# Kernel tuning notes

Measured on AMD Instinct MI355X. Metric: run time of the kernel, lower is better.

Reference implementation:

```python
import jax, jax.numpy as jnp
import numpy as np

B, C, H, W = 32, 3, 128, 128
OH, OW = 32, 32
N = OH * OW


def calc_mask(mu_x, mu_y, sigma_x, sigma_y):
    # Gaussian receptive-field mask, normalized per neuron over (C,H,W) and
    # rescaled by sqrt(C*H*W), as in AdaptiveLocal2DLayer.calc_U (channel_separate=False,
    # normed=True). The mask is identical across channels, so we keep it [H,W,N]
    # and fold the channel count C into the normalization.
    xg = jnp.linspace(0.0, 1.0, W)
    yg = jnp.linspace(0.0, 1.0, H)
    gx = jnp.exp(-0.5 * ((xg[:, None] - mu_x[None, :]) / sigma_x[None, :]) ** 2)  # [W,N]
    gy = jnp.exp(-0.5 * ((yg[:, None] - mu_y[None, :]) / sigma_y[None, :]) ** 2)  # [H,N]
    g = gy[:, None, :] * gx[None, :, :]  # [H,W,N]
    sumsq = C * jnp.sum(g * g, axis=(0, 1), keepdims=True)  # per-neuron sum over C,H,W
    return g / jnp.sqrt(sumsq) * jnp.sqrt(jnp.asarray(C * H * W, dtype=g.dtype))


def setup_inputs() -> dict:
    key = jax.random.key(0)
    kx, kw = jax.random.split(key)
    x = jax.random.normal(kx, (B, C, H, W), dtype=jnp.float32)
    # mu_init='spread': grid of centers with margin 0.2 (np.meshgrid default 'xy')
    margin = 0.2
    grid_y, grid_x = jnp.meshgrid(
        jnp.linspace(margin, 1.0 - margin, OH),
        jnp.linspace(margin, 1.0 - margin, OW),
        indexing='xy')
    mu_x = grid_x.flatten().astype(jnp.float32)
    mu_y = grid_y.flatten().astype(jnp.float32)
    sigma_x = jnp.full((N,), 0.1, dtype=jnp.float32)
    sigma_y = jnp.full((N,), 0.1, dtype=jnp.float32)
    # weight init as in the module: uniform(-bound, bound) with
    # bound = gain*sqrt(6/(eff_fan_in + fan_out)), eff_fan_in = sum(mask^2)
    mask = calc_mask(mu_x, mu_y, sigma_x, sigma_y)
    eff_fan_in = C * jnp.sum(mask ** 2)
    gain = float(np.sqrt(2.0))  # calculate_gain('relu')
    bound = gain * jnp.sqrt(6.0 / (eff_fan_in + N))
    weights = jax.random.uniform(kw, (C, H, W, N), minval=-bound, maxval=bound,
                                 dtype=jnp.float32)
    return {"x": x, "mu_x": mu_x, "mu_y": mu_y,
            "sigma_x": sigma_x, "sigma_y": sigma_y, "weights": weights}


def reference(x, mu_x, mu_y, sigma_x, sigma_y, weights):
    # forward: weighted_mask = mask * weights; tensordot over (C,H,W)
    mask = calc_mask(mu_x, mu_y, sigma_x, sigma_y)  # [H,W,N]
    wm = mask[None, :, :, :] * weights               # [C,H,W,N]
    out = jnp.einsum('bchw,chwn->bn', x, wm)         # [B,N]
    return out.reshape(x.shape[0], 1, OH, OW)
```

## Files before the change

kernel.cpp:

```cpp
#include <hip/hip_runtime.h>
#include <stdint.h>

#define BB 32
#define CC 3
#define HH 128
#define WW 128
#define NN 1024
#define KK (CC*HH*WW)
#define NROWS (CC*HH)
#define KSR NROWS
#define BH 16
#define BSPLIT (BB/BH)
#define NF4 (NN/4)
#define WCH 4
#define NCH (WW/WCH)
#define STEP (1.0f/127.0f)

__global__ void scale_kernel(const float* __restrict__ mu_x,
                             const float* __restrict__ mu_y,
                             const float* __restrict__ sigma_x,
                             const float* __restrict__ sigma_y,
                             float* __restrict__ scale) {
    int n = blockIdx.x * blockDim.x + threadIdx.x;
    if (n >= NN) return;
    float mux = mu_x[n], muy = mu_y[n];
    float isx = 1.0f / sigma_x[n], isy = 1.0f / sigma_y[n];
    float Sx = 0.f, Sy = 0.f;
    for (int i = 0; i < WW; ++i) {
        float dx = (i * STEP - mux) * isx;
        Sx += __expf(-dx * dx);
        float dy = (i * STEP - muy) * isy;
        Sy += __expf(-dy * dy);
    }
    scale[n] = sqrtf((float)(HH * WW) / (Sx * Sy));
}

__global__ void table_kernel(const float* __restrict__ mu_x,
                             const float* __restrict__ mu_y,
                             const float* __restrict__ sigma_x,
                             const float* __restrict__ sigma_y,
                             const float* __restrict__ scale,
                             float* __restrict__ gxt,
                             float* __restrict__ gyt) {
    int id = blockIdx.x * blockDim.x + threadIdx.x;
    int n = id & (NN - 1);
    int i = id >> 10;
    float sx = sigma_x[n], sy = sigma_y[n];
    float dx = i * STEP - mu_x[n];
    float dy = i * STEP - mu_y[n];
    gxt[id] = __expf(-0.5f * dx * dx / (sx * sx));
    gyt[id] = __expf(-0.5f * dy * dy / (sy * sy)) * scale[n];
}

__global__ __launch_bounds__(256) void main_pipe(
    const float* __restrict__ weights,
    const float* __restrict__ x,
    const float* __restrict__ gyt,
    const float* __restrict__ mu_x,
    const float* __restrict__ sigma_x,
    float* __restrict__ part)
{
    __shared__ float wbuf[2][WCH * NN];
    __shared__ float xtile[WW][BH];
    const int tid = threadIdx.x;

    const int d    = blockIdx.x;
    const int xcd  = d & 7;
    const int slot = d >> 3;
    const int g    = xcd * (KSR / 8) + (slot >> 1);
    const int b0   = (slot & 1) * BH;
    const int r    = g;
    const int h    = r & (HH - 1);

    {
        const int b = tid & (BH - 1);
        const int c = tid >> 4;
        const float* xp = x + (size_t)(b0 + b) * KK + (size_t)r * WW + c * 8;
        const float4 v0 = ((const float4*)xp)[0];
        const float4 v1 = ((const float4*)xp)[1];
        const int w = c * 8;
        xtile[w+0][b] = v0.x; xtile[w+1][b] = v0.y;
        xtile[w+2][b] = v0.z; xtile[w+3][b] = v0.w;
        xtile[w+4][b] = v1.x; xtile[w+5][b] = v1.y;
        xtile[w+6][b] = v1.z; xtile[w+7][b] = v1.w;
    }

    const float4 mux = ((const float4*)mu_x)[tid];
    const float4 sx  = ((const float4*)sigma_x)[tid];
    float4 ax, axs, Bf;
    ax.x = -0.5f/(sx.x*sx.x); ax.y = -0.5f/(sx.y*sx.y);
    ax.z = -0.5f/(sx.z*sx.z); ax.w = -0.5f/(sx.w*sx.w);
    axs.x = ax.x*STEP; axs.y = ax.y*STEP; axs.z = ax.z*STEP; axs.w = ax.w*STEP;
    Bf.x = __expf(2.f*axs.x*STEP); Bf.y = __expf(2.f*axs.y*STEP);
    Bf.z = __expf(2.f*axs.z*STEP); Bf.w = __expf(2.f*axs.w*STEP);

    const float4 gyrow = ((const float4*)(gyt + (size_t)h * NN))[tid];

    auto stage = [&](int c) {
        const int w0 = c * WCH;
        const float* gsrc = weights + ((size_t)r * WW + w0) * NN;
        float* lb = wbuf[c & 1];
        const int q = tid >> 6;
        const int lane = tid & 63;
#pragma unroll
        for (int i = 0; i < 4; ++i) {
            const int off = q * 1024 + i * 256;
            __builtin_amdgcn_global_load_lds(
                (const __attribute__((address_space(1))) unsigned int*)(gsrc + off + lane * 4),
                (__attribute__((address_space(3))) unsigned int*)(lb + off),
                16, 0, 0);
        }
    };

    stage(0);
    __syncthreads();

    float4 acc[BH];
#pragma unroll
    for (int b = 0; b < BH; ++b) acc[b] = make_float4(0.f, 0.f, 0.f, 0.f);

    for (int c = 0; c < NCH; ++c) {
        if (c + 1 < NCH) stage(c + 1);

        const int w0 = c * WCH;
        float4 g4, r4;
        {
            float dd;
            dd = w0*STEP - mux.x; g4.x = __expf(ax.x*dd*dd)*gyrow.x; r4.x = __expf(axs.x*(2.f*dd+STEP));
            dd = w0*STEP - mux.y; g4.y = __expf(ax.y*dd*dd)*gyrow.y; r4.y = __expf(axs.y*(2.f*dd+STEP));
            dd = w0*STEP - mux.z; g4.z = __expf(ax.z*dd*dd)*gyrow.z; r4.z = __expf(axs.z*(2.f*dd+STEP));
            dd = w0*STEP - mux.w; g4.w = __expf(ax.w*dd*dd)*gyrow.w; r4.w = __expf(axs.w*(2.f*dd+STEP));
        }

        const float* wb = wbuf[c & 1];
#pragma unroll
        for (int i = 0; i < WCH; ++i) {
            const float4 wt = *(const float4*)(wb + i * NN + (tid << 2));
            const float4* tr = (const float4*)&xtile[w0 + i][0];
            float4 t;
            t.x = g4.x * wt.x; t.y = g4.y * wt.y;
            t.z = g4.z * wt.z; t.w = g4.w * wt.w;
#pragma unroll
            for (int q = 0; q < 4; ++q) {
                const float4 xv = tr[q];
                acc[4*q+0].x = fmaf(xv.x, t.x, acc[4*q+0].x);
                acc[4*q+0].y = fmaf(xv.x, t.y, acc[4*q+0].y);
                acc[4*q+0].z = fmaf(xv.x, t.z, acc[4*q+0].z);
                acc[4*q+0].w = fmaf(xv.x, t.w, acc[4*q+0].w);
                acc[4*q+1].x = fmaf(xv.y, t.x, acc[4*q+1].x);
                acc[4*q+1].y = fmaf(xv.y, t.y, acc[4*q+1].y);
                acc[4*q+1].z = fmaf(xv.y, t.z, acc[4*q+1].z);
                acc[4*q+1].w = fmaf(xv.y, t.w, acc[4*q+1].w);
                acc[4*q+2].x = fmaf(xv.z, t.x, acc[4*q+2].x);
                acc[4*q+2].y = fmaf(xv.z, t.y, acc[4*q+2].y);
                acc[4*q+2].z = fmaf(xv.z, t.z, acc[4*q+2].z);
                acc[4*q+2].w = fmaf(xv.z, t.w, acc[4*q+2].w);
                acc[4*q+3].x = fmaf(xv.w, t.x, acc[4*q+3].x);
                acc[4*q+3].y = fmaf(xv.w, t.y, acc[4*q+3].y);
                acc[4*q+3].z = fmaf(xv.w, t.z, acc[4*q+3].z);
                acc[4*q+3].w = fmaf(xv.w, t.w, acc[4*q+3].w);
            }
            g4.x *= r4.x; g4.y *= r4.y; g4.z *= r4.z; g4.w *= r4.w;
            r4.x *= Bf.x; r4.y *= Bf.y; r4.z *= Bf.z; r4.w *= Bf.w;
        }
        __syncthreads();
    }

    float* pp = part + ((size_t)g * BB + b0) * NN + (tid << 2);
#pragma unroll
    for (int b = 0; b < BH; ++b)
        *(float4*)(pp + (size_t)b * NN) = acc[b];
}

template <int KSS>
__global__ __launch_bounds__(256) void reduce_kernel(const float* __restrict__ part,
                                                     float* __restrict__ out) {
    __shared__ float buf[256];
    const int t = threadIdx.x;
    const int half = t >> 7;
    const int cell = blockIdx.x * 128 + (t & 127);
    const int s0 = half * (KSS / 2);
    float a = 0.f;
#pragma unroll 8
    for (int s = 0; s < KSS / 2; ++s)
        a += part[(size_t)(s0 + s) * (BB * NN) + cell];
    buf[t] = a;
    __syncthreads();
    if (t < 128) out[cell] = buf[t] + buf[t + 128];
}

template <int MODE>
__global__ __launch_bounds__(256) void main_fallback(
    const float* __restrict__ weights,
    const float* __restrict__ x,
    const float* __restrict__ gxt,
    const float* __restrict__ gyt,
    const float* __restrict__ mu_x, const float* __restrict__ mu_y,
    const float* __restrict__ sigma_x, const float* __restrict__ sigma_y,
    float* __restrict__ dst)
{
    __shared__ float tile[2][WW][8];
    const int tid = threadIdx.x;
    const int g   = blockIdx.x;
    const int b0  = blockIdx.y * 8;
    const int r0  = g * 2;

    {
        const int b = tid & 7;
        const int c = tid >> 3;
        const float* xp = x + (size_t)(b0 + b) * KK + (size_t)r0 * WW + c * 8;
        const float4 v0 = ((const float4*)xp)[0];
        const float4 v1 = ((const float4*)xp)[1];
        const int row = (c * 8) >> 7;
        const int w   = (c * 8) & (WW - 1);
        tile[row][w+0][b] = v0.x; tile[row][w+1][b] = v0.y;
        tile[row][w+2][b] = v0.z; tile[row][w+3][b] = v0.w;
        tile[row][w+4][b] = v1.x; tile[row][w+5][b] = v1.y;
        tile[row][w+6][b] = v1.z; tile[row][w+7][b] = v1.w;
    }

    float4 mux4, ax4, ay4, muy4, sc4;
    if constexpr (MODE == 2) {
        mux4 = ((const float4*)mu_x)[tid];
        muy4 = ((const float4*)mu_y)[tid];
        float4 sx4 = ((const float4*)sigma_x)[tid];
        float4 sy4 = ((const float4*)sigma_y)[tid];
        ax4.x=-0.5f/(sx4.x*sx4.x); ax4.y=-0.5f/(sx4.y*sx4.y);
        ax4.z=-0.5f/(sx4.z*sx4.z); ax4.w=-0.5f/(sx4.w*sx4.w);
        ay4.x=-0.5f/(sy4.x*sy4.x); ay4.y=-0.5f/(sy4.y*sy4.y);
        ay4.z=-0.5f/(sy4.z*sy4.z); ay4.w=-0.5f/(sy4.w*sy4.w);
        float Sx[4]={0,0,0,0}, Sy[4]={0,0,0,0};
        for (int i = 0; i < WW; ++i) {
            float pp = i * STEP, dd;
            dd=pp-mux4.x; Sx[0]+=__expf(2.f*ax4.x*dd*dd);
            dd=pp-mux4.y; Sx[1]+=__expf(2.f*ax4.y*dd*dd);
            dd=pp-mux4.z; Sx[2]+=__expf(2.f*ax4.z*dd*dd);
            dd=pp-mux4.w; Sx[3]+=__expf(2.f*ax4.w*dd*dd);
            dd=pp-muy4.x; Sy[0]+=__expf(2.f*ay4.x*dd*dd);
            dd=pp-muy4.y; Sy[1]+=__expf(2.f*ay4.y*dd*dd);
            dd=pp-muy4.z; Sy[2]+=__expf(2.f*ay4.z*dd*dd);
            dd=pp-muy4.w; Sy[3]+=__expf(2.f*ay4.w*dd*dd);
        }
        sc4.x = sqrtf((float)(HH*WW)/(Sx[0]*Sy[0]));
        sc4.y = sqrtf((float)(HH*WW)/(Sx[1]*Sy[1]));
        sc4.z = sqrtf((float)(HH*WW)/(Sx[2]*Sy[2]));
        sc4.w = sqrtf((float)(HH*WW)/(Sx[3]*Sy[3]));
    }
    __syncthreads();

    float acc[8][4];
#pragma unroll
    for (int b = 0; b < 8; ++b)
        acc[b][0] = acc[b][1] = acc[b][2] = acc[b][3] = 0.f;

#pragma unroll
    for (int rr = 0; rr < 2; ++rr) {
        const int rrow = r0 + rr;
        const int hh = rrow & (HH - 1);
        float4 gys;
        if constexpr (MODE == 2) {
            float hp = hh * STEP, dd;
            dd=hp-muy4.x; gys.x = __expf(ay4.x*dd*dd) * sc4.x;
            dd=hp-muy4.y; gys.y = __expf(ay4.y*dd*dd) * sc4.y;
            dd=hp-muy4.z; gys.z = __expf(ay4.z*dd*dd) * sc4.z;
            dd=hp-muy4.w; gys.w = __expf(ay4.w*dd*dd) * sc4.w;
        } else {
            gys = ((const float4*)(gyt + (size_t)hh * NN))[tid];
        }
        const float4* wp  = (const float4*)(weights + (size_t)rrow * WW * NN) + tid;
        const float4* gxp = (const float4*)gxt + tid;
        float racc[8][4];
#pragma unroll
        for (int b = 0; b < 8; ++b)
            racc[b][0] = racc[b][1] = racc[b][2] = racc[b][3] = 0.f;
        auto GX = [&](int w) -> float4 {
            if constexpr (MODE == 2) {
                float pp = w * STEP, dd;
                float4 gg;
                dd=pp-mux4.x; gg.x = __expf(ax4.x*dd*dd);
                dd=pp-mux4.y; gg.y = __expf(ax4.y*dd*dd);
                dd=pp-mux4.z; gg.z = __expf(ax4.z*dd*dd);
                dd=pp-mux4.w; gg.w = __expf(ax4.w*dd*dd);
                return gg;
            } else {
                return gxp[(size_t)w * NF4];
            }
        };
#define COMPUTE(WIDX, WT, GXV)                                          \
        {                                                               \
            float4 t;                                                   \
            t.x = GXV.x * WT.x; t.y = GXV.y * WT.y;                     \
            t.z = GXV.z * WT.z; t.w = GXV.w * WT.w;                     \
            const float4* tr = (const float4*)&tile[rr][WIDX][0];       \
            float xs[8];                                                \
            ((float4*)xs)[0] = tr[0]; ((float4*)xs)[1] = tr[1];         \
            _Pragma("unroll")                                           \
            for (int b = 0; b < 8; ++b) {                               \
                racc[b][0] = fmaf(xs[b], t.x, racc[b][0]);              \
                racc[b][1] = fmaf(xs[b], t.y, racc[b][1]);              \
                racc[b][2] = fmaf(xs[b], t.z, racc[b][2]);              \
                racc[b][3] = fmaf(xs[b], t.w, racc[b][3]);              \
            }                                                           \
        }
        float4 wtA = wp[0];
        float4 gxA = GX(0);
        float4 wtB = wp[NF4];
        float4 gxB = GX(1);
        for (int w = 0; w < WW; w += 2) {
            const int wn = (w + 2 < WW) ? (w + 2) : (WW - 2);
            float4 wtA2 = wp[(size_t)wn * NF4];
            float4 gxA2 = GX(wn);
            float4 wtB2 = wp[(size_t)(wn + 1) * NF4];
            float4 gxB2 = GX(wn + 1);
            COMPUTE(w,     wtA, gxA);
            COMPUTE(w + 1, wtB, gxB);
            wtA = wtA2; gxA = gxA2; wtB = wtB2; gxB = gxB2;
        }
#undef COMPUTE
#pragma unroll
        for (int b = 0; b < 8; ++b) {
            acc[b][0] = fmaf(gys.x, racc[b][0], acc[b][0]);
            acc[b][1] = fmaf(gys.y, racc[b][1], acc[b][1]);
            acc[b][2] = fmaf(gys.z, racc[b][2], acc[b][2]);
            acc[b][3] = fmaf(gys.w, racc[b][3], acc[b][3]);
        }
    }

    float* op = dst + (size_t)b0 * NN + tid * 4;
#pragma unroll
    for (int b = 0; b < 8; ++b) {
        atomicAdd(op + (size_t)b * NN + 0, acc[b][0]);
        atomicAdd(op + (size_t)b * NN + 1, acc[b][1]);
        atomicAdd(op + (size_t)b * NN + 2, acc[b][2]);
        atomicAdd(op + (size_t)b * NN + 3, acc[b][3]);
    }
}

extern "C" void kernel_launch(void* const* d_in, const int* in_sizes, int n_in,
                              void* d_out, int out_size, void* d_ws, size_t ws_size,
                              hipStream_t stream) {
    const float* x       = (const float*)d_in[0];
    const float* mu_x    = (const float*)d_in[1];
    const float* mu_y    = (const float*)d_in[2];
    const float* sigma_x = (const float*)d_in[3];
    const float* sigma_y = (const float*)d_in[4];
    const float* weights = (const float*)d_in[5];
    float* out = (float*)d_out;

    float* scale = (float*)d_ws;
    float* gxt   = (float*)((char*)d_ws + 4096);
    float* gyt   = gxt + (size_t)HH * NN;
    float* part  = gyt + (size_t)HH * NN;
    const size_t need_tbl  = 4096 + 2 * sizeof(float) * (size_t)HH * NN;
    const size_t need_part = need_tbl + sizeof(float) * (size_t)KSR * BB * NN;

    if (ws_size >= need_part) {
        scale_kernel<<<(NN + 255) / 256, 256, 0, stream>>>(mu_x, mu_y, sigma_x, sigma_y, scale);
        table_kernel<<<(HH * NN) / 256, 256, 0, stream>>>(mu_x, mu_y, sigma_x, sigma_y,
                                                          scale, gxt, gyt);
        main_pipe<<<KSR * BSPLIT, 256, 0, stream>>>(weights, x, gyt, mu_x, sigma_x, part);
        reduce_kernel<KSR><<<BB * NN / 128, 256, 0, stream>>>(part, out);
    } else if (ws_size >= need_tbl) {
        hipMemsetAsync(d_out, 0, (size_t)out_size * sizeof(float), stream);
        scale_kernel<<<(NN + 255) / 256, 256, 0, stream>>>(mu_x, mu_y, sigma_x, sigma_y, scale);
        table_kernel<<<(HH * NN) / 256, 256, 0, stream>>>(mu_x, mu_y, sigma_x, sigma_y,
                                                          scale, gxt, gyt);
        dim3 grid(NROWS / 2, 4);
        main_fallback<1><<<grid, 256, 0, stream>>>(weights, x, gxt, gyt,
                                                   mu_x, mu_y, sigma_x, sigma_y, out);
    } else {
        hipMemsetAsync(d_out, 0, (size_t)out_size * sizeof(float), stream);
        dim3 grid(NROWS / 2, 4);
        main_fallback<2><<<grid, 256, 0, stream>>>(weights, x, nullptr, nullptr,
                                                   mu_x, mu_y, sigma_x, sigma_y, out);
    }
}
```

Before: 83.00 us.

## Make weight staging per-wave, drop block barriers, split reduction into two stages

Each wave now streams its own 256-column slice of the weight rows into a private LDS double buffer. It waits with explicit vmcnt counts instead of block-wide __syncthreads, which removes the per-chunk barrier from the main loop. The Gaussian x-factor is recomputed with exp only every 16 columns and advanced by the recurrence in between, so more error can accumulate along that chain. The single long reduction over 384 partial slabs becomes a two-pass float4 reduction through an extra workspace buffer. The barrier-free scheme depends on the hand-placed waitcnt values being correct.

Result: faster. 78.91 us (-4.9%).

```diff
diff --git a/kernel.cpp b/kernel.cpp
--- a/kernel.cpp
+++ b/kernel.cpp
@@ -14,6 +14,7 @@
 #define NF4 (NN/4)
 #define WCH 4
 #define NCH (WW/WCH)
+#define SG 8
 #define STEP (1.0f/127.0f)
 
 __global__ void scale_kernel(const float* __restrict__ mu_x,
@@ -60,9 +61,11 @@
     const float* __restrict__ sigma_x,
     float* __restrict__ part)
 {
-    __shared__ float wbuf[2][WCH * NN];
+    __shared__ float wbuf[4][2][WCH][256];
     __shared__ float xtile[WW][BH];
-    const int tid = threadIdx.x;
+    const int tid  = threadIdx.x;
+    const int wv   = tid >> 6;
+    const int lane = tid & 63;
 
     const int d    = blockIdx.x;
     const int xcd  = d & 7;
@@ -96,46 +99,51 @@
 
     const float4 gyrow = ((const float4*)(gyt + (size_t)h * NN))[tid];
 
+    const float* wrow = weights + (size_t)r * WW * NN + wv * 256 + lane * 4;
     auto stage = [&](int c) {
-        const int w0 = c * WCH;
-        const float* gsrc = weights + ((size_t)r * WW + w0) * NN;
-        float* lb = wbuf[c & 1];
-        const int q = tid >> 6;
-        const int lane = tid & 63;
-#pragma unroll
-        for (int i = 0; i < 4; ++i) {
-            const int off = q * 1024 + i * 256;
+        const float* gsrc = wrow + (size_t)(c * WCH) * NN;
+        float* lb = &wbuf[wv][c & 1][0][0];
+#pragma unroll
+        for (int i = 0; i < WCH; ++i) {
             __builtin_amdgcn_global_load_lds(
-                (const __attribute__((address_space(1))) unsigned int*)(gsrc + off + lane * 4),
-                (__attribute__((address_space(3))) unsigned int*)(lb + off),
+                (const __attribute__((address_space(1))) unsigned int*)(gsrc + (size_t)i * NN),
+                (__attribute__((address_space(3))) unsigned int*)(lb + i * 256),
                 16, 0, 0);
         }
     };
 
+    __syncthreads();
     stage(0);
-    __syncthreads();
 
     float4 acc[BH];
 #pragma unroll
     for (int b = 0; b < BH; ++b) acc[b] = make_float4(0.f, 0.f, 0.f, 0.f);
 
+    float4 g4, r4;
     for (int c = 0; c < NCH; ++c) {
         if (c + 1 < NCH) stage(c + 1);
 
+        if ((c & 3) == 0) {
+            const float w0s = (float)(c * WCH) * STEP;
+            float dd;
+            dd = w0s - mux.x; g4.x = __expf(ax.x*dd*dd)*gyrow.x; r4.x = __expf(axs.x*(2.f*dd+STEP));
+            dd = w0s - mux.y; g4.y = __expf(ax.y*dd*dd)*gyrow.y; r4.y = __expf(axs.y*(2.f*dd+STEP));
+            dd = w0s - mux.z; g4.z = __expf(ax.z*dd*dd)*gyrow.z; r4.z = __expf(axs.z*(2.f*dd+STEP));
+            dd = w0s - mux.w; g4.w = __expf(ax.w*dd*dd)*gyrow.w; r4.w = __expf(axs.w*(2.f*dd+STEP));
+        }
+
+        if (c + 1 < NCH) {
+            asm volatile("s_waitcnt vmcnt(4)" ::: "memory");
+        } else {
+            asm volatile("s_waitcnt vmcnt(0)" ::: "memory");
+        }
+        __builtin_amdgcn_sched_barrier(0);
+
+        const float* wb = &wbuf[wv][c & 1][0][0];
         const int w0 = c * WCH;
-        float4 g4, r4;
-        {
-            float dd;
-            dd = w0*STEP - mux.x; g4.x = __expf(ax.x*dd*dd)*gyrow.x; r4.x = __expf(axs.x*(2.f*dd+STEP));
-            dd = w0*STEP - mux.y; g4.y = __expf(ax.y*dd*dd)*gyrow.y; r4.y = __expf(axs.y*(2.f*dd+STEP));
-            dd = w0*STEP - mux.z; g4.z = __expf(ax.z*dd*dd)*gyrow.z; r4.z = __expf(axs.z*(2.f*dd+STEP));
-            dd = w0*STEP - mux.w; g4.w = __expf(ax.w*dd*dd)*gyrow.w; r4.w = __expf(axs.w*(2.f*dd+STEP));
-        }
-
-        const float* wb = wbuf[c & 1];
 #pragma unroll
         for (int i = 0; i < WCH; ++i) {
-            const float4 wt = *(const float4*)(wb + i * NN + (tid << 2));
+            const float4 wt = *(const float4*)(wb + i * 256 + (lane << 2));
             const float4* tr = (const float4*)&xtile[w0 + i][0];
             float4 t;
             t.x = g4.x * wt.x; t.y = g4.y * wt.y;
@@ -163,7 +171,6 @@
             g4.x *= r4.x; g4.y *= r4.y; g4.z *= r4.z; g4.w *= r4.w;
             r4.x *= Bf.x; r4.y *= Bf.y; r4.z *= Bf.z; r4.w *= Bf.w;
         }
-        __syncthreads();
     }
 
     float* pp = part + ((size_t)g * BB + b0) * NN + (tid << 2);
@@ -172,21 +179,30 @@
         *(float4*)(pp + (size_t)b * NN) = acc[b];
 }
 
-template <int KSS>
-__global__ __launch_bounds__(256) void reduce_kernel(const float* __restrict__ part,
-                                                     float* __restrict__ out) {
-    __shared__ float buf[256];
-    const int t = threadIdx.x;
-    const int half = t >> 7;
-    const int cell = blockIdx.x * 128 + (t & 127);
-    const int s0 = half * (KSS / 2);
-    float a = 0.f;
-#pragma unroll 8
-    for (int s = 0; s < KSS / 2; ++s)
-        a += part[(size_t)(s0 + s) * (BB * NN) + cell];
-    buf[t] = a;
-    __syncthreads();
-    if (t < 128) out[cell] = buf[t] + buf[t + 128];
+__global__ __launch_bounds__(256) void reduce1_kernel(const float* __restrict__ part,
+                                                      float* __restrict__ part2) {
+    const int sg = blockIdx.x >> 5;
+    const int cq = (blockIdx.x & 31) * 256 + threadIdx.x;
+    const int s0 = sg * (KSR / SG);
+    float4 a = make_float4(0.f, 0.f, 0.f, 0.f);
+#pragma unroll 4
+    for (int s = 0; s < KSR / SG; ++s) {
+        const float4 v = *(const float4*)(part + (size_t)(s0 + s) * (BB * NN) + cq * 4);
+        a.x += v.x; a.y += v.y; a.z += v.z; a.w += v.w;
+    }
+    *(float4*)(part2 + ((size_t)sg * (BB * NN) + cq * 4)) = a;
+}
+
+__global__ __launch_bounds__(256) void reduce2_kernel(const float* __restrict__ part2,
+                                                      float* __restrict__ out) {
+    const int cq = blockIdx.x * 256 + threadIdx.x;
+    float4 a = make_float4(0.f, 0.f, 0.f, 0.f);
+#pragma unroll
+    for (int sgi = 0; sgi < SG; ++sgi) {
+        const float4 v = *(const float4*)(part2 + (size_t)sgi * (BB * NN) + cq * 4);
+        a.x += v.x; a.y += v.y; a.z += v.z; a.w += v.w;
+    }
+    *(float4*)(out + cq * 4) = a;
 }
 
 template <int MODE>
@@ -291,9 +307,9 @@
             float4 t;                                                   \
             t.x = GXV.x * WT.x; t.y = GXV.y * WT.y;                     \
             t.z = GXV.z * WT.z; t.w = GXV.w * WT.w;                     \
-            const float4* tr = (const float4*)&tile[rr][WIDX][0];       \
+            const float4* trp = (const float4*)&tile[rr][WIDX][0];      \
             float xs[8];                                                \
-            ((float4*)xs)[0] = tr[0]; ((float4*)xs)[1] = tr[1];         \
+            ((float4*)xs)[0] = trp[0]; ((float4*)xs)[1] = trp[1];       \
             _Pragma("unroll")                                           \
             for (int b = 0; b < 8; ++b) {                               \
                 racc[b][0] = fmaf(xs[b], t.x, racc[b][0]);              \
@@ -351,15 +367,18 @@
     float* gxt   = (float*)((char*)d_ws + 4096);
     float* gyt   = gxt + (size_t)HH * NN;
     float* part  = gyt + (size_t)HH * NN;
+    float* part2 = part + (size_t)KSR * BB * NN;
     const size_t need_tbl  = 4096 + 2 * sizeof(float) * (size_t)HH * NN;
-    const size_t need_part = need_tbl + sizeof(float) * (size_t)KSR * BB * NN;
+    const size_t need_part = need_tbl +
+        sizeof(float) * ((size_t)KSR * BB * NN + (size_t)SG * BB * NN);
 
     if (ws_size >= need_part) {
         scale_kernel<<<(NN + 255) / 256, 256, 0, stream>>>(mu_x, mu_y, sigma_x, sigma_y, scale);
         table_kernel<<<(HH * NN) / 256, 256, 0, stream>>>(mu_x, mu_y, sigma_x, sigma_y,
                                                           scale, gxt, gyt);
         main_pipe<<<KSR * BSPLIT, 256, 0, stream>>>(weights, x, gyt, mu_x, sigma_x, part);
-        reduce_kernel<KSR><<<BB * NN / 128, 256, 0, stream>>>(part, out);
+        reduce1_kernel<<<32 * SG, 256, 0, stream>>>(part, part2);
+        reduce2_kernel<<<BB * NN / 4 / 256, 256, 0, stream>>>(part2, out);
     } else if (ws_size >= need_tbl) {
         hipMemsetAsync(d_out, 0, (size_t)out_size * sizeof(float), stream);
         scale_kernel<<<(NN + 255) / 256, 256, 0, stream>>>(mu_x, mu_y, sigma_x, sigma_y, scale);
```
